# Optimization experiments

Measured on AMD Instinct MI355X. Metric: run time of the kernel, lower is better.

The kernel has to match this reference:

```python
import jax, jax.numpy as jnp
import numpy as np

B, S, D, H = 4, 2048, 1024, 16
DQKV = max(1, D // H)  # 64


def setup_inputs() -> dict:
    key = jax.random.key(0)
    ks = jax.random.split(key, 12)
    std = 1.0 / np.sqrt(D)
    inp = {
        "query": jax.random.normal(ks[0], (B, S, D), dtype=jnp.float32),
        "key": jax.random.normal(ks[1], (B, S, D), dtype=jnp.float32),
        "value": jax.random.normal(ks[2], (B, S, D), dtype=jnp.float32),
        # per-head projection weights, stacked over heads: [H, DQKV, D] (torch Linear layout [out,in])
        "wq": jax.random.uniform(ks[3], (H, DQKV, D), jnp.float32, -std, std),
        "bq": jax.random.uniform(ks[4], (H, DQKV), jnp.float32, -std, std),
        "wk": jax.random.uniform(ks[5], (H, DQKV, D), jnp.float32, -std, std),
        "bk": jax.random.uniform(ks[6], (H, DQKV), jnp.float32, -std, std),
        "wv": jax.random.uniform(ks[7], (H, DQKV, D), jnp.float32, -std, std),
        "bv": jax.random.uniform(ks[8], (H, DQKV), jnp.float32, -std, std),
        # output projection: [D, H*DQKV]
        "wo": jax.random.uniform(ks[9], (D, H * DQKV), jnp.float32, -1.0 / np.sqrt(H * DQKV), 1.0 / np.sqrt(H * DQKV)),
        "bo": jax.random.uniform(ks[10], (D,), jnp.float32, -1.0 / np.sqrt(H * DQKV), 1.0 / np.sqrt(H * DQKV)),
    }
    return inp


def reference(query, key, value, wq, bq, wk, bk, wv, bv, wo, bo):
    # Per-head linear projections (batched over heads): [B, H, S, DQKV]
    Q = jnp.einsum("bsd,hed->bhse", query, wq) + bq[None, :, None, :]
    K = jnp.einsum("bsd,hed->bhse", key, wk) + bk[None, :, None, :]
    V = jnp.einsum("bsd,hed->bhse", value, wv) + bv[None, :, None, :]
    scale = jnp.asarray(DQKV, Q.dtype) ** 0.5
    # Full N x N attention scores per head (matches naive bmm+softmax+bmm)
    scores = jnp.einsum("bhse,bhte->bhst", Q, K) / scale
    attn = jax.nn.softmax(scores, axis=-1)
    ctx = jnp.einsum("bhst,bhte->bhse", attn, V)  # [B, H, S, DQKV]
    # Concat over heads in head-major order: [B, S, H*DQKV]
    concat = jnp.transpose(ctx, (0, 2, 1, 3)).reshape(ctx.shape[0], ctx.shape[2], H * DQKV)
    return jnp.einsum("bsf,df->bsd", concat, wo) + bo
```

## Files before the change

### kernel.cpp

```cpp
#include <hip/hip_runtime.h>
#include <stdint.h>
#include <stddef.h>


typedef __attribute__((ext_vector_type(8))) short short8;
typedef __attribute__((ext_vector_type(4))) float f32x4;

#if __has_builtin(__builtin_amdgcn_exp2f)
#define EXP2F __builtin_amdgcn_exp2f
#else
#define EXP2F exp2f
#endif
#if __has_builtin(__builtin_amdgcn_rcpf)
#define RCPF __builtin_amdgcn_rcpf
#else
#define RCPF(x) (1.0f / (x))
#endif

__device__ __forceinline__ uint16_t f2bf(float f) {
  uint32_t u = __builtin_bit_cast(uint32_t, f);
  u += 0x7FFFu + ((u >> 16) & 1u);
  return (uint16_t)(u >> 16);
}

__device__ __forceinline__ void gld16(const void* g, void* l) {
  __builtin_amdgcn_global_load_lds((const __attribute__((address_space(1))) void*)g,
                                   (__attribute__((address_space(3))) void*)l, 16, 0, 0);
}

__global__ __launch_bounds__(256) void cast3(const float* __restrict__ s0, const float* __restrict__ s1,
                                             const float* __restrict__ s2, uint16_t* __restrict__ d0,
                                             uint16_t* __restrict__ d1, uint16_t* __restrict__ d2,
                                             int n4) {
  const int z = blockIdx.y;
  const float* s = z == 0 ? s0 : (z == 1 ? s1 : s2);
  uint16_t* d = z == 0 ? d0 : (z == 1 ? d1 : d2);
  int i = blockIdx.x * 256 + threadIdx.x;
  if (i >= n4) return;
  float4 v = ((const float4*)s)[i];
  ushort4 o;
  o.x = f2bf(v.x); o.y = f2bf(v.y); o.z = f2bf(v.z); o.w = f2bf(v.w);
  ((ushort4*)d)[i] = o;
}

__global__ __launch_bounds__(256) void cast4(const float* __restrict__ s0, const float* __restrict__ s1,
                                             const float* __restrict__ s2, const float* __restrict__ s3,
                                             uint16_t* __restrict__ d0, uint16_t* __restrict__ d1,
                                             uint16_t* __restrict__ d2, uint16_t* __restrict__ d3,
                                             int n4) {
  const int z = blockIdx.y;
  const float* s = z == 0 ? s0 : (z == 1 ? s1 : (z == 2 ? s2 : s3));
  uint16_t* d = z == 0 ? d0 : (z == 1 ? d1 : (z == 2 ? d2 : d3));
  int i = blockIdx.x * 256 + threadIdx.x;
  if (i >= n4) return;
  float4 v = ((const float4*)s)[i];
  ushort4 o;
  o.x = f2bf(v.x); o.y = f2bf(v.y); o.z = f2bf(v.z); o.w = f2bf(v.w);
  ((ushort4*)d)[i] = o;
}

__device__ __forceinline__ void gemm_stage(const uint16_t* const* Ag, const uint16_t* const* Bg,
                                           const int* lofs, uint16_t* As, uint16_t* Bs, int k0) {
#pragma unroll
  for (int c = 0; c < 4; ++c) {
    gld16(Ag[c] + k0, As + lofs[c]);
    gld16(Bg[c] + k0, Bs + lofs[c]);
  }
}

__device__ __forceinline__ void gemm_compute(const uint16_t* As, const uint16_t* Bs,
                                             f32x4 acc[4][4], int wm, int wn, int ln, int quad,
                                             const int* colk) {
#pragma unroll
  for (int kk = 0; kk < 2; ++kk) {
    short8 a[4], b[4];
#pragma unroll
    for (int mt = 0; mt < 4; ++mt)
      a[mt] = *(const short8*)(As + (wm + mt * 16 + ln) * 64 + colk[kk] * 8);
#pragma unroll
    for (int nt = 0; nt < 4; ++nt)
      b[nt] = *(const short8*)(Bs + (wn + nt * 16 + ln) * 64 + colk[kk] * 8);
#pragma unroll
    for (int mt = 0; mt < 4; ++mt)
#pragma unroll
      for (int nt = 0; nt < 4; ++nt)
        acc[mt][nt] = __builtin_amdgcn_mfma_f32_16x16x32_bf16(a[mt], b[nt], acc[mt][nt], 0, 0, 0);
  }
}

__device__ __forceinline__ void gemm_core(const uint16_t* __restrict__ A,
                                          const uint16_t* __restrict__ Bw,
                                          uint16_t* As0, uint16_t* Bs0,
                                          uint16_t* As1, uint16_t* Bs1,
                                          f32x4 acc[4][4], int m0, int n0) {
  constexpr int K = 1024;
  const int tid = threadIdx.x;
  const int w = tid >> 6, l = tid & 63;
  const int ln = l & 15, quad = l >> 4;
  const int wm = (w >> 1) * 64, wn = (w & 1) * 64;

  const uint16_t* Ag[4];
  const uint16_t* Bg[4];
  int lofs[4];
#pragma unroll
  for (int c = 0; c < 4; ++c) {
    const int f = c * 256 + tid;
    const int row = f >> 3, cp = f & 7, g = (cp - row) & 7;
    Ag[c] = A + (size_t)(m0 + row) * K + g * 8;
    Bg[c] = Bw + (size_t)(n0 + row) * K + g * 8;
    lofs[c] = f * 8;
  }
  int colk[2];
#pragma unroll
  for (int kk = 0; kk < 2; ++kk) colk[kk] = (kk * 4 + quad + ln) & 7;

  gemm_stage(Ag, Bg, lofs, As0, Bs0, 0);
  __syncthreads();
#pragma unroll
  for (int s = 0; s < 16; ++s) {
    uint16_t* Asn = (s & 1) ? As0 : As1;
    uint16_t* Bsn = (s & 1) ? Bs0 : Bs1;
    const uint16_t* Asc = (s & 1) ? As1 : As0;
    const uint16_t* Bsc = (s & 1) ? Bs1 : Bs0;
    if (s < 15) gemm_stage(Ag, Bg, lofs, Asn, Bsn, (s + 1) * 64);
    gemm_compute(Asc, Bsc, acc, wm, wn, ln, quad, colk);
    if (s < 15) __syncthreads();
  }
}

__global__ __launch_bounds__(256) void gemm_qkv(const uint16_t* __restrict__ Xq, const uint16_t* __restrict__ Xk,
                                                const uint16_t* __restrict__ Xv, const uint16_t* __restrict__ Wq,
                                                const uint16_t* __restrict__ Wk, const uint16_t* __restrict__ Wv,
                                                const float* __restrict__ bq, const float* __restrict__ bk,
                                                const float* __restrict__ bv, uint16_t* __restrict__ Qb,
                                                uint16_t* __restrict__ Kb, uint16_t* __restrict__ Vtb,
                                                float qscale, int zbase) {
  __shared__ __attribute__((aligned(16))) uint16_t As0[128 * 64];
  __shared__ __attribute__((aligned(16))) uint16_t Bs0[128 * 64];
  __shared__ __attribute__((aligned(16))) uint16_t As1[128 * 64];
  __shared__ __attribute__((aligned(16))) uint16_t Bs1[128 * 64];
  const int lin = blockIdx.x + (blockIdx.y << 3) + (blockIdx.z << 9);
  const int per = gridDim.z << 3;
  const int xcd = lin & 7, local = lin >> 3;
  const int mz = xcd * per + (local >> 3);
  const int z = (mz >> 6) + zbase;
  const int m0 = (mz & 63) * 128, n0 = (local & 7) * 128;

  const uint16_t* A = z == 0 ? Xq : (z == 1 ? Xk : Xv);
  const uint16_t* Bw = z == 0 ? Wq : (z == 1 ? Wk : Wv);
  const float* bias = z == 0 ? bq : (z == 1 ? bk : bv);
  uint16_t* Cout = z == 0 ? Qb : (z == 1 ? Kb : Vtb);
  const float scale = z == 0 ? qscale : 1.0f;

  f32x4 acc[4][4] = {};
  gemm_core(A, Bw, As0, Bs0, As1, Bs1, acc, m0, n0);

  const int tid = threadIdx.x;
  const int w = tid >> 6, l = tid & 63;
  const int ln = l & 15, quad = l >> 4;
  const int wm = (w >> 1) * 64, wn = (w & 1) * 64;
#pragma unroll
  for (int nt = 0; nt < 4; ++nt) {
    const int col = n0 + wn + nt * 16 + ln;
    const float bv_ = bias[col];
    const int h = col >> 6, e = col & 63;
#pragma unroll
    for (int mt = 0; mt < 4; ++mt) {
#pragma unroll
      for (int i = 0; i < 4; ++i) {
        const int row = m0 + wm + mt * 16 + quad * 4 + i;
        const int b_ = row >> 11, s = row & 2047;
        const float v = (acc[mt][nt][i] + bv_) * scale;
        if (z != 2) {
          Cout[(size_t)(b_ * 16 + h) * 131072 + s * 64 + e] = f2bf(v);
        } else {
          Cout[(size_t)(b_ * 16 + h) * 131072 + e * 2048 + s] = f2bf(v);
        }
      }
    }
  }
}

__global__ __launch_bounds__(256) void gemm_out(const uint16_t* __restrict__ A, const uint16_t* __restrict__ Bw,
                                                const float* __restrict__ bias, float* __restrict__ Cout) {
  __shared__ __attribute__((aligned(16))) uint16_t As0[128 * 64];
  __shared__ __attribute__((aligned(16))) uint16_t Bs0[128 * 64];
  __shared__ __attribute__((aligned(16))) uint16_t As1[128 * 64];
  __shared__ __attribute__((aligned(16))) uint16_t Bs1[128 * 64];
  const int lin = blockIdx.x + (blockIdx.y << 3);
  const int xcd = lin & 7, local = lin >> 3;
  const int m0 = (xcd * 8 + (local >> 3)) * 128, n0 = (local & 7) * 128;
  f32x4 acc[4][4] = {};
  gemm_core(A, Bw, As0, Bs0, As1, Bs1, acc, m0, n0);

  const int tid = threadIdx.x;
  const int w = tid >> 6, l = tid & 63;
  const int ln = l & 15, quad = l >> 4;
  const int wm = (w >> 1) * 64, wn = (w & 1) * 64;
#pragma unroll
  for (int nt = 0; nt < 4; ++nt) {
    const int col = n0 + wn + nt * 16 + ln;
    const float bv_ = bias[col];
#pragma unroll
    for (int mt = 0; mt < 4; ++mt)
#pragma unroll
      for (int i = 0; i < 4; ++i) {
        const int row = m0 + wm + mt * 16 + quad * 4 + i;
        Cout[(size_t)row * 1024 + col] = acc[mt][nt][i] + bv_;
      }
  }
}

__global__ __launch_bounds__(256, 4) void attn(const uint16_t* __restrict__ Qb,
                                               const uint16_t* __restrict__ Kb,
                                               const uint16_t* __restrict__ Vtb,
                                               uint16_t* __restrict__ Ctx) {
  __shared__ __attribute__((aligned(16))) uint16_t Ks[64 * 64];
  __shared__ __attribute__((aligned(16))) uint16_t Vs[64 * 64];
  __shared__ __attribute__((aligned(16))) uint16_t Ps[4 * 2 * 16 * 72];
  const int tid = threadIdx.x;
  const int w = tid >> 6, l = tid & 63;
  const int ln = l & 15, quad = l >> 4;
  const int lin = blockIdx.x + (blockIdx.y << 4);
  const int slot = lin >> 3;
  const int bh = (lin & 7) * 8 + (slot >> 4);
  const int q0 = (slot & 15) * 128;
  const int b = bh >> 4, h = bh & 15;
  const uint16_t* Qh = Qb + (size_t)bh * 131072;
  const uint16_t* Kh = Kb + (size_t)bh * 131072;
  const uint16_t* Vth = Vtb + (size_t)bh * 131072;

  short8 qf[2][2];
#pragma unroll
  for (int sub = 0; sub < 2; ++sub)
#pragma unroll
    for (int ks = 0; ks < 2; ++ks)
      qf[sub][ks] = *(const short8*)(Qh + (size_t)(q0 + w * 32 + sub * 16 + ln) * 64 + ks * 32 + quad * 8);

  short8 ones;
#pragma unroll
  for (int j = 0; j < 8; ++j) ones[j] = (short)0x3F80;

  int col[2];
#pragma unroll
  for (int ks = 0; ks < 2; ++ks) col[ks] = (ks * 4 + quad + ln) & 7;
  uint16_t* Pw = Ps + w * 2304;

  f32x4 oacc[2][4] = {};
  f32x4 lacc[2] = {};

  for (int t0 = 0; t0 < 2048; t0 += 64) {
    __syncthreads();
#pragma unroll
    for (int c = 0; c < 2; ++c) {
      const int f = w * 128 + c * 64 + l;
      const int t = f >> 3, g = ((f & 7) - t) & 7;
      gld16(Kh + (size_t)(t0 + t) * 64 + g * 8, Ks + (w * 128 + c * 64) * 8);
      gld16(Vth + (size_t)t * 2048 + t0 + g * 8, Vs + (w * 128 + c * 64) * 8);
    }
    __syncthreads();

    f32x4 sacc[2][4] = {};
    __builtin_amdgcn_s_setprio(1);
#pragma unroll
    for (int nt = 0; nt < 4; ++nt) {
      const int t = nt * 16 + ln;
#pragma unroll
      for (int ks = 0; ks < 2; ++ks) {
        const short8 kf = *(const short8*)(Ks + (t * 8 + col[ks]) * 8);
        sacc[0][nt] = __builtin_amdgcn_mfma_f32_16x16x32_bf16(kf, qf[0][ks], sacc[0][nt], 0, 0, 0);
        sacc[1][nt] = __builtin_amdgcn_mfma_f32_16x16x32_bf16(kf, qf[1][ks], sacc[1][nt], 0, 0, 0);
      }
    }
    __builtin_amdgcn_s_setprio(0);

#pragma unroll
    for (int sub = 0; sub < 2; ++sub)
#pragma unroll
      for (int nt = 0; nt < 4; ++nt) {
        const uint32_t u0 = __builtin_bit_cast(uint32_t, EXP2F(sacc[sub][nt][0]));
        const uint32_t u1 = __builtin_bit_cast(uint32_t, EXP2F(sacc[sub][nt][1]));
        const uint32_t u2 = __builtin_bit_cast(uint32_t, EXP2F(sacc[sub][nt][2]));
        const uint32_t u3 = __builtin_bit_cast(uint32_t, EXP2F(sacc[sub][nt][3]));
        uint2 dd;
        dd.x = ((u0 + 0x7FFFu + ((u0 >> 16) & 1u)) >> 16) |
               ((u1 + 0x7FFFu + ((u1 >> 16) & 1u)) & 0xFFFF0000u);
        dd.y = ((u2 + 0x7FFFu + ((u2 >> 16) & 1u)) >> 16) |
               ((u3 + 0x7FFFu + ((u3 >> 16) & 1u)) & 0xFFFF0000u);
        *(uint2*)(Pw + sub * 1152 + ln * 72 + nt * 16 + quad * 4) = dd;
      }

#pragma unroll
    for (int ks = 0; ks < 2; ++ks) {
      const short8 pf0 = *(const short8*)(Pw + ln * 72 + ks * 32 + quad * 8);
      const short8 pf1 = *(const short8*)(Pw + 1152 + ln * 72 + ks * 32 + quad * 8);
      __builtin_amdgcn_s_setprio(1);
      lacc[0] = __builtin_amdgcn_mfma_f32_16x16x32_bf16(pf0, ones, lacc[0], 0, 0, 0);
      lacc[1] = __builtin_amdgcn_mfma_f32_16x16x32_bf16(pf1, ones, lacc[1], 0, 0, 0);
#pragma unroll
      for (int nt = 0; nt < 4; ++nt) {
        const int e = nt * 16 + ln;
        const short8 vf = *(const short8*)(Vs + (e * 8 + col[ks]) * 8);
        oacc[0][nt] = __builtin_amdgcn_mfma_f32_16x16x32_bf16(pf0, vf, oacc[0][nt], 0, 0, 0);
        oacc[1][nt] = __builtin_amdgcn_mfma_f32_16x16x32_bf16(pf1, vf, oacc[1][nt], 0, 0, 0);
      }
      __builtin_amdgcn_s_setprio(0);
    }
  }

#pragma unroll
  for (int sub = 0; sub < 2; ++sub) {
    float inv[4];
#pragma unroll
    for (int i = 0; i < 4; ++i) inv[i] = RCPF(lacc[sub][i]);
#pragma unroll
    for (int nt = 0; nt < 4; ++nt)
#pragma unroll
      for (int i = 0; i < 4; ++i) {
        const float v = oacc[sub][nt][i] * inv[i];
        const int s = q0 + w * 32 + sub * 16 + quad * 4 + i;
        Ctx[(size_t)(b * 2048 + s) * 1024 + h * 64 + nt * 16 + ln] = f2bf(v);
      }
  }
}

extern "C" void kernel_launch(void* const* d_in, const int* in_sizes, int n_in,
                              void* d_out, int out_size, void* d_ws, size_t ws_size,
                              hipStream_t stream) {
  const float* q = (const float*)d_in[0];
  const float* k = (const float*)d_in[1];
  const float* v = (const float*)d_in[2];
  const float* wq = (const float*)d_in[3];
  const float* bq = (const float*)d_in[4];
  const float* wk = (const float*)d_in[5];
  const float* bk = (const float*)d_in[6];
  const float* wv = (const float*)d_in[7];
  const float* bv = (const float*)d_in[8];
  const float* wo = (const float*)d_in[9];
  const float* bo = (const float*)d_in[10];
  float* out = (float*)d_out;

  uint16_t* ws = (uint16_t*)d_ws;
  uint16_t* Xq = ws;
  uint16_t* Xk = Xq + 8388608;
  uint16_t* Xv = Xk + 8388608;
  uint16_t* Wq = Xv + 8388608;
  uint16_t* Wk = Wq + 1048576;
  uint16_t* Wv = Wk + 1048576;
  uint16_t* Wo = Wv + 1048576;
  uint16_t* Qb = Wo + 1048576;
  uint16_t* Kb = Qb + 8388608;
  uint16_t* Ctx = Xq;

  const size_t fused_elems = 46137344u + 8388608u;
  const bool fused = ws_size >= fused_elems * sizeof(uint16_t);
  uint16_t* Vtb = fused ? (Kb + 8388608) : Xk;

  cast3<<<dim3(8192, 3), 256, 0, stream>>>(q, k, v, Xq, Xk, Xv, 2097152);
  cast4<<<dim3(1024, 4), 256, 0, stream>>>(wq, wk, wv, wo, Wq, Wk, Wv, Wo, 262144);

  const float qscale = 0.125f * 1.4426950408889634f;
  if (fused) {
    gemm_qkv<<<dim3(8, 64, 3), 256, 0, stream>>>(Xq, Xk, Xv, Wq, Wk, Wv, bq, bk, bv,
                                                 Qb, Kb, Vtb, qscale, 0);
  } else {
    gemm_qkv<<<dim3(8, 64, 1), 256, 0, stream>>>(Xq, Xk, Xv, Wq, Wk, Wv, bq, bk, bv,
                                                 Qb, Kb, Vtb, qscale, 0);
    gemm_qkv<<<dim3(8, 64, 1), 256, 0, stream>>>(Xq, Xk, Xv, Wq, Wk, Wv, bq, bk, bv,
                                                 Qb, Kb, Vtb, qscale, 1);
    gemm_qkv<<<dim3(8, 64, 1), 256, 0, stream>>>(Xq, Xk, Xv, Wq, Wk, Wv, bq, bk, bv,
                                                 Qb, Kb, Vtb, qscale, 2);
  }

  attn<<<dim3(16, 64), 256, 0, stream>>>(Qb, Kb, Vtb, Ctx);

  gemm_out<<<dim3(8, 64), 256, 0, stream>>>(Ctx, Wo, bo, out);
}
```

Before: 370.9 us.

## Merge cast kernels, single-buffer output GEMM, use perm for bf16 packing

Folds the separate activation and weight cast kernels into one launch, cutting one kernel launch and its tail. The output-projection GEMM switches from double-buffered to single-buffered shared memory, which halves its LDS footprint and may raise occupancy, but it loses load/compute overlap. The attention softmax packs bf16 pairs with a byte-permute builtin instead of separate shift/and/or operations.

```diff
diff --git a/kernel.cpp b/kernel.cpp
--- a/kernel.cpp
+++ b/kernel.cpp
@@ -23,40 +23,65 @@
   return (uint16_t)(u >> 16);
 }
 
+__device__ __forceinline__ uint32_t pack_hi16(uint32_t r0, uint32_t r1) {
+#if __has_builtin(__builtin_amdgcn_perm)
+  return __builtin_amdgcn_perm(r1, r0, 0x07060302u);
+#else
+  return (r0 >> 16) | (r1 & 0xFFFF0000u);
+#endif
+}
+
 __device__ __forceinline__ void gld16(const void* g, void* l) {
   __builtin_amdgcn_global_load_lds((const __attribute__((address_space(1))) void*)g,
                                    (__attribute__((address_space(3))) void*)l, 16, 0, 0);
 }
 
-__global__ __launch_bounds__(256) void cast3(const float* __restrict__ s0, const float* __restrict__ s1,
-                                             const float* __restrict__ s2, uint16_t* __restrict__ d0,
-                                             uint16_t* __restrict__ d1, uint16_t* __restrict__ d2,
-                                             int n4) {
-  const int z = blockIdx.y;
-  const float* s = z == 0 ? s0 : (z == 1 ? s1 : s2);
-  uint16_t* d = z == 0 ? d0 : (z == 1 ? d1 : d2);
+__global__ __launch_bounds__(256) void castAll(const float* __restrict__ x0, const float* __restrict__ x1,
+                                               const float* __restrict__ x2, const float* __restrict__ w0,
+                                               const float* __restrict__ w1, const float* __restrict__ w2,
+                                               const float* __restrict__ w3, uint16_t* __restrict__ dx0,
+                                               uint16_t* __restrict__ dx1, uint16_t* __restrict__ dx2,
+                                               uint16_t* __restrict__ dw0, uint16_t* __restrict__ dw1,
+                                               uint16_t* __restrict__ dw2, uint16_t* __restrict__ dw3) {
+  const int y = blockIdx.y;
   int i = blockIdx.x * 256 + threadIdx.x;
-  if (i >= n4) return;
+  const float* s;
+  uint16_t* d;
+  if (y < 3) {
+    if (i >= 2097152) return;
+    s = y == 0 ? x0 : (y == 1 ? x1 : x2);
+    d = y == 0 ? dx0 : (y == 1 ? dx1 : dx2);
+  } else {
+    if (i >= 1048576) return;
+    const int sub = i >> 18;
+    i &= 262143;
+    s = sub == 0 ? w0 : (sub == 1 ? w1 : (sub == 2 ? w2 : w3));
+    d = sub == 0 ? dw0 : (sub == 1 ? dw1 : (sub == 2 ? dw2 : dw3));
+  }
   float4 v = ((const float4*)s)[i];
   ushort4 o;
   o.x = f2bf(v.x); o.y = f2bf(v.y); o.z = f2bf(v.z); o.w = f2bf(v.w);
   ((ushort4*)d)[i] = o;
 }
 
-__global__ __launch_bounds__(256) void cast4(const float* __restrict__ s0, const float* __restrict__ s1,
-                                             const float* __restrict__ s2, const float* __restrict__ s3,
-                                             uint16_t* __restrict__ d0, uint16_t* __restrict__ d1,
-                                             uint16_t* __restrict__ d2, uint16_t* __restrict__ d3,
-                                             int n4) {
-  const int z = blockIdx.y;
-  const float* s = z == 0 ? s0 : (z == 1 ? s1 : (z == 2 ? s2 : s3));
-  uint16_t* d = z == 0 ? d0 : (z == 1 ? d1 : (z == 2 ? d2 : d3));
-  int i = blockIdx.x * 256 + threadIdx.x;
-  if (i >= n4) return;
-  float4 v = ((const float4*)s)[i];
-  ushort4 o;
-  o.x = f2bf(v.x); o.y = f2bf(v.y); o.z = f2bf(v.z); o.w = f2bf(v.w);
-  ((ushort4*)d)[i] = o;
+__device__ __forceinline__ void gemm_compute(const uint16_t* As, const uint16_t* Bs,
+                                             f32x4 acc[4][4], int wm, int wn, int ln, int quad,
+                                             const int* colk) {
+#pragma unroll
+  for (int kk = 0; kk < 2; ++kk) {
+    short8 a[4], b[4];
+#pragma unroll
+    for (int mt = 0; mt < 4; ++mt)
+      a[mt] = *(const short8*)(As + (wm + mt * 16 + ln) * 64 + colk[kk] * 8);
+#pragma unroll
+    for (int nt = 0; nt < 4; ++nt)
+      b[nt] = *(const short8*)(Bs + (wn + nt * 16 + ln) * 64 + colk[kk] * 8);
+#pragma unroll
+    for (int mt = 0; mt < 4; ++mt)
+#pragma unroll
+      for (int nt = 0; nt < 4; ++nt)
+        acc[mt][nt] = __builtin_amdgcn_mfma_f32_16x16x32_bf16(a[mt], b[nt], acc[mt][nt], 0, 0, 0);
+  }
 }
 
 __device__ __forceinline__ void gemm_stage(const uint16_t* const* Ag, const uint16_t* const* Bg,
@@ -68,40 +93,14 @@
   }
 }
 
-__device__ __forceinline__ void gemm_compute(const uint16_t* As, const uint16_t* Bs,
-                                             f32x4 acc[4][4], int wm, int wn, int ln, int quad,
-                                             const int* colk) {
-#pragma unroll
-  for (int kk = 0; kk < 2; ++kk) {
-    short8 a[4], b[4];
-#pragma unroll
-    for (int mt = 0; mt < 4; ++mt)
-      a[mt] = *(const short8*)(As + (wm + mt * 16 + ln) * 64 + colk[kk] * 8);
-#pragma unroll
-    for (int nt = 0; nt < 4; ++nt)
-      b[nt] = *(const short8*)(Bs + (wn + nt * 16 + ln) * 64 + colk[kk] * 8);
-#pragma unroll
-    for (int mt = 0; mt < 4; ++mt)
-#pragma unroll
-      for (int nt = 0; nt < 4; ++nt)
-        acc[mt][nt] = __builtin_amdgcn_mfma_f32_16x16x32_bf16(a[mt], b[nt], acc[mt][nt], 0, 0, 0);
-  }
-}
-
-__device__ __forceinline__ void gemm_core(const uint16_t* __restrict__ A,
-                                          const uint16_t* __restrict__ Bw,
-                                          uint16_t* As0, uint16_t* Bs0,
-                                          uint16_t* As1, uint16_t* Bs1,
-                                          f32x4 acc[4][4], int m0, int n0) {
+__device__ __forceinline__ void gemm_prolog(const uint16_t* __restrict__ A,
+                                            const uint16_t* __restrict__ Bw,
+                                            const uint16_t** Ag, const uint16_t** Bg, int* lofs,
+                                            int* colk, int m0, int n0) {
   constexpr int K = 1024;
   const int tid = threadIdx.x;
-  const int w = tid >> 6, l = tid & 63;
-  const int ln = l & 15, quad = l >> 4;
-  const int wm = (w >> 1) * 64, wn = (w & 1) * 64;
-
-  const uint16_t* Ag[4];
-  const uint16_t* Bg[4];
-  int lofs[4];
+  const int l = tid & 63;
+  const int ln = l & 15, quad = l >> 4;
 #pragma unroll
   for (int c = 0; c < 4; ++c) {
     const int f = c * 256 + tid;
@@ -110,9 +109,23 @@
     Bg[c] = Bw + (size_t)(n0 + row) * K + g * 8;
     lofs[c] = f * 8;
   }
-  int colk[2];
 #pragma unroll
   for (int kk = 0; kk < 2; ++kk) colk[kk] = (kk * 4 + quad + ln) & 7;
+}
+
+__device__ __forceinline__ void gemm_core_db(const uint16_t* __restrict__ A,
+                                             const uint16_t* __restrict__ Bw,
+                                             uint16_t* As0, uint16_t* Bs0,
+                                             uint16_t* As1, uint16_t* Bs1,
+                                             f32x4 acc[4][4], int m0, int n0) {
+  const int tid = threadIdx.x;
+  const int w = tid >> 6, l = tid & 63;
+  const int ln = l & 15, quad = l >> 4;
+  const int wm = (w >> 1) * 64, wn = (w & 1) * 64;
+  const uint16_t* Ag[4];
+  const uint16_t* Bg[4];
+  int lofs[4], colk[2];
+  gemm_prolog(A, Bw, Ag, Bg, lofs, colk, m0, n0);
 
   gemm_stage(Ag, Bg, lofs, As0, Bs0, 0);
   __syncthreads();
@@ -125,6 +138,27 @@
     if (s < 15) gemm_stage(Ag, Bg, lofs, Asn, Bsn, (s + 1) * 64);
     gemm_compute(Asc, Bsc, acc, wm, wn, ln, quad, colk);
     if (s < 15) __syncthreads();
+  }
+}
+
+__device__ __forceinline__ void gemm_core_sb(const uint16_t* __restrict__ A,
+                                             const uint16_t* __restrict__ Bw,
+                                             uint16_t* As, uint16_t* Bs,
+                                             f32x4 acc[4][4], int m0, int n0) {
+  const int tid = threadIdx.x;
+  const int w = tid >> 6, l = tid & 63;
+  const int ln = l & 15, quad = l >> 4;
+  const int wm = (w >> 1) * 64, wn = (w & 1) * 64;
+  const uint16_t* Ag[4];
+  const uint16_t* Bg[4];
+  int lofs[4], colk[2];
+  gemm_prolog(A, Bw, Ag, Bg, lofs, colk, m0, n0);
+
+  for (int k0 = 0; k0 < 1024; k0 += 64) {
+    __syncthreads();
+    gemm_stage(Ag, Bg, lofs, As, Bs, k0);
+    __syncthreads();
+    gemm_compute(As, Bs, acc, wm, wn, ln, quad, colk);
   }
 }
 
@@ -153,7 +187,7 @@
   const float scale = z == 0 ? qscale : 1.0f;
 
   f32x4 acc[4][4] = {};
-  gemm_core(A, Bw, As0, Bs0, As1, Bs1, acc, m0, n0);
+  gemm_core_db(A, Bw, As0, Bs0, As1, Bs1, acc, m0, n0);
 
   const int tid = threadIdx.x;
   const int w = tid >> 6, l = tid & 63;
@@ -183,15 +217,13 @@
 
 __global__ __launch_bounds__(256) void gemm_out(const uint16_t* __restrict__ A, const uint16_t* __restrict__ Bw,
                                                 const float* __restrict__ bias, float* __restrict__ Cout) {
-  __shared__ __attribute__((aligned(16))) uint16_t As0[128 * 64];
-  __shared__ __attribute__((aligned(16))) uint16_t Bs0[128 * 64];
-  __shared__ __attribute__((aligned(16))) uint16_t As1[128 * 64];
-  __shared__ __attribute__((aligned(16))) uint16_t Bs1[128 * 64];
+  __shared__ __attribute__((aligned(16))) uint16_t As[128 * 64];
+  __shared__ __attribute__((aligned(16))) uint16_t Bs[128 * 64];
   const int lin = blockIdx.x + (blockIdx.y << 3);
   const int xcd = lin & 7, local = lin >> 3;
   const int m0 = (xcd * 8 + (local >> 3)) * 128, n0 = (local & 7) * 128;
   f32x4 acc[4][4] = {};
-  gemm_core(A, Bw, As0, Bs0, As1, Bs1, acc, m0, n0);
+  gemm_core_sb(A, Bw, As, Bs, acc, m0, n0);
 
   const int tid = threadIdx.x;
   const int w = tid >> 6, l = tid & 63;
@@ -282,11 +314,13 @@
         const uint32_t u1 = __builtin_bit_cast(uint32_t, EXP2F(sacc[sub][nt][1]));
         const uint32_t u2 = __builtin_bit_cast(uint32_t, EXP2F(sacc[sub][nt][2]));
         const uint32_t u3 = __builtin_bit_cast(uint32_t, EXP2F(sacc[sub][nt][3]));
+        const uint32_t r0 = u0 + 0x7FFFu + ((u0 >> 16) & 1u);
+        const uint32_t r1 = u1 + 0x7FFFu + ((u1 >> 16) & 1u);
+        const uint32_t r2 = u2 + 0x7FFFu + ((u2 >> 16) & 1u);
+        const uint32_t r3 = u3 + 0x7FFFu + ((u3 >> 16) & 1u);
         uint2 dd;
-        dd.x = ((u0 + 0x7FFFu + ((u0 >> 16) & 1u)) >> 16) |
-               ((u1 + 0x7FFFu + ((u1 >> 16) & 1u)) & 0xFFFF0000u);
-        dd.y = ((u2 + 0x7FFFu + ((u2 >> 16) & 1u)) >> 16) |
-               ((u3 + 0x7FFFu + ((u3 >> 16) & 1u)) & 0xFFFF0000u);
+        dd.x = pack_hi16(r0, r1);
+        dd.y = pack_hi16(r2, r3);
         *(uint2*)(Pw + sub * 1152 + ln * 72 + nt * 16 + quad * 4) = dd;
       }
 
@@ -356,8 +390,8 @@
   const bool fused = ws_size >= fused_elems * sizeof(uint16_t);
   uint16_t* Vtb = fused ? (Kb + 8388608) : Xk;
 
-  cast3<<<dim3(8192, 3), 256, 0, stream>>>(q, k, v, Xq, Xk, Xv, 2097152);
-  cast4<<<dim3(1024, 4), 256, 0, stream>>>(wq, wk, wv, wo, Wq, Wk, Wv, Wo, 262144);
+  castAll<<<dim3(8192, 4), 256, 0, stream>>>(q, k, v, wq, wk, wv, wo,
+                                             Xq, Xk, Xv, Wq, Wk, Wv, Wo);
 
   const float qscale = 0.125f * 1.4426950408889634f;
   if (fused) {
```

Result: faster. 347.0 us (-6.4%).
